# Optimization experiments

Measured on AMD Instinct MI355X. Metric: run time of the kernel, lower is better.

## Reference

```python
import jax, jax.numpy as jnp
import numpy as np

N, M = 8192, 128
EPS = 1e-4


def setup_inputs() -> dict:
    key = jax.random.key(0)
    k1, k2, k3 = jax.random.split(key, 3)
    out1 = jax.random.normal(k1, (N, M), dtype=jnp.float32)
    out2 = jax.random.normal(k2, (N, M), dtype=jnp.float32)
    label = jax.random.uniform(k3, (N, N), dtype=jnp.float32)
    return {"out1": out1, "out2": out2, "label": label}


def _dir_loss(a, b, mob):
    # pairwise_inner_product(a, b) in the torch code equals b @ a.T:
    # inner[i, j] = <b[i], a[j]>
    scores = jnp.einsum('im,jm->ij', b, a)          # [n, n]
    phat = jax.nn.softmax(scores, axis=-1)
    return jnp.sum(-mob * jnp.log(phat + EPS))


def reference(out1, out2, label):
    loss = _dir_loss(out1, out2, label)
    loss = loss + _dir_loss(out2, out1, label.T)
    return loss
```

## Files before the change

### kernel.cpp

```cpp
#include <hip/hip_runtime.h>
#include <hip/hip_bf16.h>

#define NN 8192
#define MM 128
#define EPSF 1e-4f
#define SHIFT 30.0f

typedef __bf16 bf16x8 __attribute__((ext_vector_type(8)));
typedef __bf16 bf16x4 __attribute__((ext_vector_type(4)));
typedef float floatx4 __attribute__((ext_vector_type(4)));

__global__ void convert_kernel(const float* __restrict__ in0,
                               const float* __restrict__ in1,
                               __bf16* __restrict__ o0,
                               __bf16* __restrict__ o1) {
    const float* in = blockIdx.y ? in1 : in0;
    __bf16* out = blockIdx.y ? o1 : o0;
    int i = (blockIdx.x * blockDim.x + threadIdx.x) * 4;
    float4 v = *reinterpret_cast<const float4*>(in + i);
    bf16x4 o = { (__bf16)v.x, (__bf16)v.y, (__bf16)v.z, (__bf16)v.w };
    *reinterpret_cast<bf16x4*>(out + i) = o;
}

#define LOAD_A(dst, ptr)                                                   \
    do {                                                                   \
        dst[0] = *reinterpret_cast<const bf16x8*>((ptr) + 0);              \
        dst[1] = *reinterpret_cast<const bf16x8*>((ptr) + 32);             \
        dst[2] = *reinterpret_cast<const bf16x8*>((ptr) + 64);             \
        dst[3] = *reinterpret_cast<const bf16x8*>((ptr) + 96);             \
    } while (0)

__global__ __launch_bounds__(256)
void sums_kernel(const __bf16* __restrict__ A, const __bf16* __restrict__ B,
                 float* __restrict__ sums) {
    const int tid = threadIdx.x;
    const int w = tid >> 6, lane = tid & 63, q = lane >> 4, ln = lane & 15;
    const int i0 = blockIdx.y * 128 + w * 32;
    const int jbase = blockIdx.x * 512;

    const floatx4 accInit = {-SHIFT, -SHIFT, -SHIFT, -SHIFT};

    bf16x8 a[2][4];
    #pragma unroll
    for (int rg = 0; rg < 2; ++rg)
        LOAD_A(a[rg], A + (size_t)(i0 + rg * 16 + ln) * MM + q * 8);

    float p[2][4] = {{0.f, 0.f, 0.f, 0.f}, {0.f, 0.f, 0.f, 0.f}};

    for (int js = 0; js < 8; ++js) {
        const int j0 = jbase + js * 64;
        bf16x8 b[4][4];
        #pragma unroll
        for (int cg = 0; cg < 4; ++cg)
            LOAD_A(b[cg], B + (size_t)(j0 + cg * 16 + ln) * MM + q * 8);
        #pragma unroll
        for (int cg = 0; cg < 4; ++cg) {
            floatx4 acc0 = accInit, acc1 = accInit;
            #pragma unroll
            for (int k = 0; k < 4; ++k) {
                acc0 = __builtin_amdgcn_mfma_f32_16x16x32_bf16(a[0][k], b[cg][k], acc0, 0, 0, 0);
                acc1 = __builtin_amdgcn_mfma_f32_16x16x32_bf16(a[1][k], b[cg][k], acc1, 0, 0, 0);
            }
            float e0[4], e1[4];
            #pragma unroll
            for (int r = 0; r < 4; ++r) {
                e0[r] = __expf(acc0[r]);
                e1[r] = __expf(acc1[r]);
                p[0][r] += e0[r];
                p[1][r] += e1[r];
            }
            float c = ((e0[0] + e0[1]) + (e0[2] + e0[3])) +
                      ((e1[0] + e1[1]) + (e1[2] + e1[3]));
            c += __shfl_xor(c, 16);
            c += __shfl_xor(c, 32);
            if (q == 0) atomicAdd(&sums[NN + j0 + cg * 16 + ln], c);
        }
    }

    #pragma unroll
    for (int m = 1; m <= 8; m <<= 1)
        #pragma unroll
        for (int rg = 0; rg < 2; ++rg)
            #pragma unroll
            for (int r = 0; r < 4; ++r)
                p[rg][r] += __shfl_xor(p[rg][r], m);
    if (ln == 0)
        #pragma unroll
        for (int rg = 0; rg < 2; ++rg)
            #pragma unroll
            for (int r = 0; r < 4; ++r)
                atomicAdd(&sums[i0 + rg * 16 + q * 4 + r], p[rg][r]);
}

__global__ void recip_kernel(const float* __restrict__ s, float* __restrict__ r) {
    int i = blockIdx.x * 256 + threadIdx.x;
    r[i] = 1.0f / s[i];
}

__global__ __launch_bounds__(256)
void loss_kernel(const __bf16* __restrict__ A, const __bf16* __restrict__ B,
                 const float* __restrict__ lrowR, const float* __restrict__ lcolR,
                 const float* __restrict__ label, float* __restrict__ out) {
    const int tid = threadIdx.x;
    const int w = tid >> 6, lane = tid & 63, q = lane >> 4, ln = lane & 15;
    const int i0 = blockIdx.y * 128 + w * 32;
    const int jbase = blockIdx.x * 256;

    const floatx4 accInit = {-SHIFT, -SHIFT, -SHIFT, -SHIFT};

    bf16x8 a[2][4];
    float rl[2];
    const float* labp[2];
    #pragma unroll
    for (int rg = 0; rg < 2; ++rg) {
        const int row = i0 + rg * 16 + ln;
        LOAD_A(a[rg], A + (size_t)row * MM + q * 8);
        rl[rg] = lrowR[row];
        labp[rg] = label + (size_t)row * NN;
    }

    float lacc = 0.f;
    #pragma unroll
    for (int js = 0; js < 4; ++js) {
        const int j0 = jbase + js * 64;
        floatx4 rc[4], lb[2][4];
        #pragma unroll
        for (int cg = 0; cg < 4; ++cg) {
            const int c4 = j0 + cg * 16 + q * 4;
            rc[cg] = *reinterpret_cast<const floatx4*>(&lcolR[c4]);
            lb[0][cg] = *reinterpret_cast<const floatx4*>(&labp[0][c4]);
            lb[1][cg] = *reinterpret_cast<const floatx4*>(&labp[1][c4]);
        }
        #pragma unroll
        for (int cg = 0; cg < 4; ++cg) {
            const __bf16* br = B + (size_t)(j0 + cg * 16 + ln) * MM + q * 8;
            bf16x8 b[4];
            LOAD_A(b, br);
            floatx4 acc0 = accInit, acc1 = accInit;
            #pragma unroll
            for (int k = 0; k < 4; ++k) {
                acc0 = __builtin_amdgcn_mfma_f32_16x16x32_bf16(b[k], a[0][k], acc0, 0, 0, 0);
                acc1 = __builtin_amdgcn_mfma_f32_16x16x32_bf16(b[k], a[1][k], acc1, 0, 0, 0);
            }
            #pragma unroll
            for (int r = 0; r < 4; ++r) {
                float e0 = __expf(acc0[r]);
                float t0 = __logf(fmaf(e0, rl[0], EPSF) * fmaf(e0, rc[cg][r], EPSF));
                lacc = fmaf(lb[0][cg][r], t0, lacc);
                float e1 = __expf(acc1[r]);
                float t1 = __logf(fmaf(e1, rl[1], EPSF) * fmaf(e1, rc[cg][r], EPSF));
                lacc = fmaf(lb[1][cg][r], t1, lacc);
            }
        }
    }

    #pragma unroll
    for (int m = 1; m <= 32; m <<= 1) lacc += __shfl_xor(lacc, m);
    __shared__ float red[4];
    if (lane == 0) red[w] = lacc;
    __syncthreads();
    if (tid == 0) atomicAdd(out, -((red[0] + red[1]) + (red[2] + red[3])));
}

extern "C" void kernel_launch(void* const* d_in, const int* in_sizes, int n_in,
                              void* d_out, int out_size, void* d_ws, size_t ws_size,
                              hipStream_t stream) {
    const float* out1 = (const float*)d_in[0];
    const float* out2 = (const float*)d_in[1];
    const float* label = (const float*)d_in[2];

    char* ws = (char*)d_ws;
    __bf16* out1b = (__bf16*)ws;
    __bf16* out2b = (__bf16*)(ws + (size_t)(2 << 20));
    float* sums   = (float*)(ws + (size_t)(4 << 20));
    float* recips = sums + 2 * NN;

    hipMemsetAsync(sums, 0, 2 * NN * sizeof(float), stream);
    hipMemsetAsync(d_out, 0, sizeof(float), stream);

    convert_kernel<<<dim3(1024, 2), 256, 0, stream>>>(out1, out2, out1b, out2b);

    sums_kernel<<<dim3(16, 64), 256, 0, stream>>>(out2b, out1b, sums);
    recip_kernel<<<dim3(64), 256, 0, stream>>>(sums, recips);

    loss_kernel<<<dim3(32, 64), 256, 0, stream>>>(out2b, out1b,
                                                  recips,
                                                  recips + NN,
                                                  label, (float*)d_out);
}
```

Baseline: 458.9 us.

## Prefetch label into L2 during sums pass, stage B in swizzled LDS

Three changes. The sums kernel now issues global-to-LDS loads of the whole label matrix into a throwaway LDS buffer, so the 256 MB label is pulled into cache while the first pass is compute-bound. The loss kernel stages its 128-column B tile in XOR-swizzled shared memory and halves the column span per block, doubling the grid. The two memsets are folded into the convert kernel. The prefetch only helps if label stays resident in L2/MALL until the loss pass reads it. It also adds memory traffic that competes with the sums pass.

Result: no change. 451.7 us (-1.6%).

```diff
diff --git a/kernel.cpp b/kernel.cpp
--- a/kernel.cpp
+++ b/kernel.cpp
@@ -1,5 +1,6 @@
 #include <hip/hip_runtime.h>
 #include <hip/hip_bf16.h>
+#include <stdint.h>
 
 #define NN 8192
 #define MM 128
@@ -10,16 +11,32 @@
 typedef __bf16 bf16x4 __attribute__((ext_vector_type(4)));
 typedef float floatx4 __attribute__((ext_vector_type(4)));
 
+__device__ __forceinline__ void pf16(const float* g, void* lds) {
+    __builtin_amdgcn_global_load_lds(
+        (__attribute__((address_space(1))) void*)(uintptr_t)g,
+        (__attribute__((address_space(3))) void*)(uint32_t)(uintptr_t)lds,
+        16, 0, 0);
+}
+
 __global__ void convert_kernel(const float* __restrict__ in0,
                                const float* __restrict__ in1,
                                __bf16* __restrict__ o0,
-                               __bf16* __restrict__ o1) {
+                               __bf16* __restrict__ o1,
+                               float* __restrict__ sums,
+                               float* __restrict__ out) {
     const float* in = blockIdx.y ? in1 : in0;
-    __bf16* out = blockIdx.y ? o1 : o0;
+    __bf16* op = blockIdx.y ? o1 : o0;
     int i = (blockIdx.x * blockDim.x + threadIdx.x) * 4;
     float4 v = *reinterpret_cast<const float4*>(in + i);
     bf16x4 o = { (__bf16)v.x, (__bf16)v.y, (__bf16)v.z, (__bf16)v.w };
-    *reinterpret_cast<bf16x4*>(out + i) = o;
+    *reinterpret_cast<bf16x4*>(op + i) = o;
+    if (blockIdx.y == 0) {
+        if (blockIdx.x < 16) {
+            floatx4 z = {0.f, 0.f, 0.f, 0.f};
+            *reinterpret_cast<floatx4*>(sums + (blockIdx.x * 256 + threadIdx.x) * 4) = z;
+        }
+        if (blockIdx.x == 16 && threadIdx.x == 0) *out = 0.f;
+    }
 }
 
 #define LOAD_A(dst, ptr)                                                   \
@@ -32,11 +49,14 @@
 
 __global__ __launch_bounds__(256)
 void sums_kernel(const __bf16* __restrict__ A, const __bf16* __restrict__ B,
-                 float* __restrict__ sums) {
+                 const float* __restrict__ label, float* __restrict__ sums) {
+    __shared__ alignas(16) char pfbuf[1024];
     const int tid = threadIdx.x;
     const int w = tid >> 6, lane = tid & 63, q = lane >> 4, ln = lane & 15;
     const int i0 = blockIdx.y * 128 + w * 32;
     const int jbase = blockIdx.x * 512;
+    const int bid = blockIdx.y * gridDim.x + blockIdx.x;
+    const float* pfb = label + (size_t)bid * 65536 + w * 2048 + lane * 4;
 
     const floatx4 accInit = {-SHIFT, -SHIFT, -SHIFT, -SHIFT};
 
@@ -53,6 +73,9 @@
         #pragma unroll
         for (int cg = 0; cg < 4; ++cg)
             LOAD_A(b[cg], B + (size_t)(j0 + cg * 16 + ln) * MM + q * 8);
+        #pragma unroll
+        for (int u = 0; u < 8; ++u)
+            pf16(pfb + js * 8192 + u * 256, pfbuf);
         #pragma unroll
         for (int cg = 0; cg < 4; ++cg) {
             floatx4 acc0 = accInit, acc1 = accInit;
@@ -101,10 +124,23 @@
 void loss_kernel(const __bf16* __restrict__ A, const __bf16* __restrict__ B,
                  const float* __restrict__ lrowR, const float* __restrict__ lcolR,
                  const float* __restrict__ label, float* __restrict__ out) {
+    __shared__ alignas(16) __bf16 Bs[128 * 128];
     const int tid = threadIdx.x;
     const int w = tid >> 6, lane = tid & 63, q = lane >> 4, ln = lane & 15;
     const int i0 = blockIdx.y * 128 + w * 32;
-    const int jbase = blockIdx.x * 256;
+    const int jbase = blockIdx.x * 128;
+
+    {
+        const bf16x8* src = reinterpret_cast<const bf16x8*>(B + (size_t)jbase * MM);
+        char* dst = reinterpret_cast<char*>(Bs);
+        #pragma unroll
+        for (int u = 0; u < 8; ++u) {
+            int ch = u * 256 + tid;
+            int row = ch >> 4, slot = ch & 15;
+            bf16x8 v = src[ch];
+            *reinterpret_cast<bf16x8*>(dst + row * 256 + ((slot ^ (row & 7)) << 4)) = v;
+        }
+    }
 
     const floatx4 accInit = {-SHIFT, -SHIFT, -SHIFT, -SHIFT};
 
@@ -118,10 +154,13 @@
         rl[rg] = lrowR[row];
         labp[rg] = label + (size_t)row * NN;
     }
-
+    __syncthreads();
+
+    const char* bsc = reinterpret_cast<const char*>(Bs);
+    const int swz = (ln & 7);
     float lacc = 0.f;
     #pragma unroll
-    for (int js = 0; js < 4; ++js) {
+    for (int js = 0; js < 2; ++js) {
         const int j0 = jbase + js * 64;
         floatx4 rc[4], lb[2][4];
         #pragma unroll
@@ -133,9 +172,12 @@
         }
         #pragma unroll
         for (int cg = 0; cg < 4; ++cg) {
-            const __bf16* br = B + (size_t)(j0 + cg * 16 + ln) * MM + q * 8;
+            const int lrow = js * 64 + cg * 16 + ln;
+            const char* bp = bsc + lrow * 256;
             bf16x8 b[4];
-            LOAD_A(b, br);
+            #pragma unroll
+            for (int k = 0; k < 4; ++k)
+                b[k] = *reinterpret_cast<const bf16x8*>(bp + (((q + 4 * k) ^ swz) << 4));
             floatx4 acc0 = accInit, acc1 = accInit;
             #pragma unroll
             for (int k = 0; k < 4; ++k) {
@@ -175,15 +217,13 @@
     float* sums   = (float*)(ws + (size_t)(4 << 20));
     float* recips = sums + 2 * NN;
 
-    hipMemsetAsync(sums, 0, 2 * NN * sizeof(float), stream);
-    hipMemsetAsync(d_out, 0, sizeof(float), stream);
-
-    convert_kernel<<<dim3(1024, 2), 256, 0, stream>>>(out1, out2, out1b, out2b);
-
-    sums_kernel<<<dim3(16, 64), 256, 0, stream>>>(out2b, out1b, sums);
+    convert_kernel<<<dim3(1024, 2), 256, 0, stream>>>(out1, out2, out1b, out2b,
+                                                      sums, (float*)d_out);
+
+    sums_kernel<<<dim3(16, 64), 256, 0, stream>>>(out2b, out1b, label, sums);
     recip_kernel<<<dim3(64), 256, 0, stream>>>(sums, recips);
 
-    loss_kernel<<<dim3(32, 64), 256, 0, stream>>>(out2b, out1b,
+    loss_kernel<<<dim3(64, 64), 256, 0, stream>>>(out2b, out1b,
                                                   recips,
                                                   recips + NN,
                                                   label, (float*)d_out);
```
